# Performance work log

Measured on AMD Instinct MI355X. Metric: run time of the kernel, lower is better.

## Reference

```python
import jax, jax.numpy as jnp
import numpy as np

EMBED_DIM = 1024
NUM_HEADS = 16
HEAD_DIM = EMBED_DIM // NUM_HEADS
TGT_LEN, BSZ = 2048, 4


def setup_inputs() -> dict:
    key = jax.random.key(0)
    ks = jax.random.split(key, 12)
    s = 1.0 / np.sqrt(EMBED_DIM)
    inp = {
        "query": jax.random.normal(ks[0], (TGT_LEN, BSZ, EMBED_DIM), jnp.float32),
        "key": jax.random.normal(ks[1], (TGT_LEN, BSZ, EMBED_DIM), jnp.float32),
        "value": jax.random.normal(ks[2], (TGT_LEN, BSZ, EMBED_DIM), jnp.float32),
        # nn.Linear weights: [out, in], y = x @ W.T + b
        "Wq": jax.random.normal(ks[3], (EMBED_DIM, EMBED_DIM), jnp.float32) * s,
        "bq": jax.random.normal(ks[4], (EMBED_DIM,), jnp.float32) * s,
        "Wk": jax.random.normal(ks[5], (EMBED_DIM, EMBED_DIM), jnp.float32) * s,
        "bk": jax.random.normal(ks[6], (EMBED_DIM,), jnp.float32) * s,
        "Wv": jax.random.normal(ks[7], (EMBED_DIM, EMBED_DIM), jnp.float32) * s,
        "bv": jax.random.normal(ks[8], (EMBED_DIM,), jnp.float32) * s,
        "Wo": jax.random.normal(ks[9], (EMBED_DIM, EMBED_DIM), jnp.float32) * s,
        "bo": jax.random.normal(ks[10], (EMBED_DIM,), jnp.float32) * s,
    }
    return inp


def _split_heads(x, seq_len, bsz):
    # [S, B, E] -> [B*H, S, Dh]
    return x.reshape(seq_len, bsz * NUM_HEADS, HEAD_DIM).transpose(1, 0, 2)


def reference(query, key, value, Wq, bq, Wk, bk, Wv, bv, Wo, bo):
    tgt_len, bsz, embed_dim = query.shape
    src_len = key.shape[0]
    q = query @ Wq.T + bq
    k = key @ Wk.T + bk
    v = value @ Wv.T + bv
    q = _split_heads(q, tgt_len, bsz)   # [B*H, T, Dh]
    k = _split_heads(k, src_len, bsz)   # [B*H, S, Dh]
    v = _split_heads(v, src_len, bsz)   # [B*H, S, Dh]
    scale = 1.0 / np.sqrt(HEAD_DIM).astype(np.float32)
    attn_weights = jnp.einsum('btd,bsd->bts', q, k) * scale  # [B*H, T, S]
    attn_weights = jax.nn.softmax(attn_weights, axis=-1)
    attn = jnp.einsum('bts,bsd->btd', attn_weights, v)       # [B*H, T, Dh]
    attn = attn.transpose(1, 0, 2).reshape(tgt_len, bsz, embed_dim)
    return attn @ Wo.T + bo
```

## Files before the change

### kernel.cpp

```cpp
#include <hip/hip_runtime.h>
#include <stdint.h>

#define TGT 2048
#define BSZQ 4
#define EMB 1024
#define NHEAD 16
#define DH 64
#define BH 64
#define MROWS 8192

using short8 = __attribute__((ext_vector_type(8))) short;
using f32x4  = __attribute__((ext_vector_type(4))) float;
using u32x4  = __attribute__((ext_vector_type(4))) unsigned int;
typedef unsigned short u16;
typedef unsigned int u32;

#define QSCALE 0.18033688011112042f

__device__ __forceinline__ u16 f2bf(float f) {
  union { float f; u32 u; } v; v.f = f;
  return (u16)((v.u + 0x7fffu + ((v.u >> 16) & 1u)) >> 16);
}
__device__ __forceinline__ u32 packbf(float a, float b) {
  union { float f; u32 u; } x, y; x.f = a; y.f = b;
  return __builtin_amdgcn_perm(y.u + 0x8000u, x.u + 0x8000u, 0x07060302u);
}
__device__ __forceinline__ f32x4 mfma16(short8 a, short8 b, f32x4 c) {
  return __builtin_amdgcn_mfma_f32_16x16x32_bf16(a, b, c, 0, 0, 0);
}
__device__ __forceinline__ void gload_lds16(const u16* g, u16* l) {
  __builtin_amdgcn_global_load_lds((const __attribute__((address_space(1))) void*)g,
                                   (__attribute__((address_space(3))) void*)l,
                                   16, 0, 0);
}

__global__ __launch_bounds__(256)
void cvt3(const float* __restrict__ a, const float* __restrict__ b, const float* __restrict__ c,
          u16* __restrict__ oa, u16* __restrict__ ob, u16* __restrict__ oc)
{
  const float* s; u16* d;
  if (blockIdx.y == 0) { s = a; d = oa; }
  else if (blockIdx.y == 1) { s = b; d = ob; }
  else { s = c; d = oc; }
  const int i = (blockIdx.x * 256 + threadIdx.x) * 8;
  float4 v0 = *(const float4*)(s + i);
  float4 v1 = *(const float4*)(s + i + 4);
  union { u16 h[8]; short8 v; } r;
  r.h[0] = f2bf(v0.x); r.h[1] = f2bf(v0.y); r.h[2] = f2bf(v0.z); r.h[3] = f2bf(v0.w);
  r.h[4] = f2bf(v1.x); r.h[5] = f2bf(v1.y); r.h[6] = f2bf(v1.z); r.h[7] = f2bf(v1.w);
  *(short8*)(d + i) = r.v;
}
__global__ __launch_bounds__(256)
void cvt4(const float* __restrict__ a, const float* __restrict__ b,
          const float* __restrict__ c, const float* __restrict__ e,
          u16* __restrict__ oa, u16* __restrict__ ob, u16* __restrict__ oc, u16* __restrict__ oe)
{
  const float* s; u16* d;
  if (blockIdx.y == 0) { s = a; d = oa; }
  else if (blockIdx.y == 1) { s = b; d = ob; }
  else if (blockIdx.y == 2) { s = c; d = oc; }
  else { s = e; d = oe; }
  const int i = (blockIdx.x * 256 + threadIdx.x) * 8;
  float4 v0 = *(const float4*)(s + i);
  float4 v1 = *(const float4*)(s + i + 4);
  union { u16 h[8]; short8 v; } r;
  r.h[0] = f2bf(v0.x); r.h[1] = f2bf(v0.y); r.h[2] = f2bf(v0.z); r.h[3] = f2bf(v0.w);
  r.h[4] = f2bf(v1.x); r.h[5] = f2bf(v1.y); r.h[6] = f2bf(v1.z); r.h[7] = f2bf(v1.w);
  *(short8*)(d + i) = r.v;
}

__device__ __forceinline__
void gemm_body(const u16* __restrict__ A, const u16* __restrict__ W,
               const float* __restrict__ bias, void* __restrict__ outp,
               u16* As, u16* Bs, int mode)
{
  const int tid = threadIdx.x;
  const int wave = tid >> 6, lane = tid & 63;
  const int wm = wave >> 1, wn = wave & 1;
  const int col16 = lane & 15, quad = lane >> 4;
  const int m0 = blockIdx.y * 128, n0 = blockIdx.x * 128;
  const int lr = lane >> 2;
  const int lc = (lane & 3) * 8;

  f32x4 acc[4][4];
#pragma unroll
  for (int i = 0; i < 4; ++i)
#pragma unroll
    for (int j = 0; j < 4; ++j) acc[i][j] = (f32x4)0.0f;

  for (int kt = 0; kt < EMB / 64; ++kt) {
    const int k0 = kt * 64;
#pragma unroll
    for (int kk = 0; kk < 2; ++kk) {
#pragma unroll
      for (int h = 0; h < 2; ++h) {
        const int rbase = wave * 32 + h * 16;
        const int r = rbase + lr;
        gload_lds16(A + (size_t)(m0 + r) * EMB + k0 + kk * 32 + lc,
                    &As[kk * 4096 + rbase * 32]);
        gload_lds16(W + (size_t)(n0 + r) * EMB + k0 + kk * 32 + lc,
                    &Bs[kk * 4096 + rbase * 32]);
      }
    }
    __syncthreads();
    short8 af[4][2], bfr[4][2];
#pragma unroll
    for (int i = 0; i < 4; ++i)
#pragma unroll
      for (int kk = 0; kk < 2; ++kk) {
        af[i][kk]  = *(const short8*)&As[kk * 4096 + (wm * 64 + i * 16 + col16) * 32 + quad * 8];
        bfr[i][kk] = *(const short8*)&Bs[kk * 4096 + (wn * 64 + i * 16 + col16) * 32 + quad * 8];
      }
#pragma unroll
    for (int i = 0; i < 4; ++i)
#pragma unroll
      for (int j = 0; j < 4; ++j) {
        acc[i][j] = mfma16(af[i][0], bfr[j][0], acc[i][j]);
        acc[i][j] = mfma16(af[i][1], bfr[j][1], acc[i][j]);
      }
    __syncthreads();
  }

  const int rowb = quad * 4;
#pragma unroll
  for (int i = 0; i < 4; ++i) {
#pragma unroll
    for (int j = 0; j < 4; ++j) {
      const int gn = n0 + wn * 64 + j * 16 + col16;
      const float bia = bias[gn];
#pragma unroll
      for (int r = 0; r < 4; ++r) {
        const int gm = m0 + wm * 64 + i * 16 + rowb + r;
        float val = acc[i][j][r] + bia;
        const int t = gm >> 2, b = gm & 3, h = gn >> 6, d = gn & 63;
        if (mode == 0) {
          ((u16*)outp)[((size_t)(b * NHEAD + h) * TGT + t) * DH + d] = f2bf(val * QSCALE);
        } else if (mode == 1) {
          ((u16*)outp)[((size_t)(b * NHEAD + h) * TGT + t) * DH + d] = f2bf(val);
        } else if (mode == 2) {
          const int p = (t & ~127) + ((t & 15) << 3) + ((t >> 4) & 7);
          ((u16*)outp)[((size_t)(b * NHEAD + h) * DH + d) * TGT + p] = f2bf(val);
        } else {
          ((float*)outp)[(size_t)gm * EMB + gn] = val;
        }
      }
    }
  }
}

__global__ __launch_bounds__(256, 2)
void gemm_qkv(const u16* __restrict__ qb, const u16* __restrict__ kb, const u16* __restrict__ vb,
              const u16* __restrict__ wq, const u16* __restrict__ wk, const u16* __restrict__ wv,
              const float* __restrict__ bq, const float* __restrict__ bk, const float* __restrict__ bv,
              u16* __restrict__ qh, u16* __restrict__ kh, u16* __restrict__ vtp)
{
  __shared__ u16 As[2 * 4096];
  __shared__ u16 Bs[2 * 4096];
  const int z = blockIdx.z;
  const u16* A = (z == 0) ? qb : (z == 1) ? kb : vb;
  const u16* W = (z == 0) ? wq : (z == 1) ? wk : wv;
  const float* bias = (z == 0) ? bq : (z == 1) ? bk : bv;
  void* outp = (z == 0) ? (void*)qh : (z == 1) ? (void*)kh : (void*)vtp;
  gemm_body(A, W, bias, outp, As, Bs, z);
}

__global__ __launch_bounds__(256, 2)
void gemm_o(const u16* __restrict__ A, const u16* __restrict__ W,
            const float* __restrict__ bias, float* __restrict__ outp)
{
  __shared__ u16 As[2 * 4096];
  __shared__ u16 Bs[2 * 4096];
  gemm_body(A, W, bias, (void*)outp, As, Bs, 3);
}

__global__ __launch_bounds__(256, 2)
void flash_attn(const u16* __restrict__ qh, const u16* __restrict__ kh,
                const u16* __restrict__ vtp, u16* __restrict__ ao)
{
  __shared__ u16 Ks[128 * 64];
  __shared__ u16 Vs[64 * 128];
  __shared__ u16 Ps[128 * 136];

  const int tid = threadIdx.x;
  const int wave = tid >> 6, lane = tid & 63;
  const int col16 = lane & 15, quad = lane >> 4;
  const int id = blockIdx.x;
  const int bh = (id & 7) * 8 + (id >> 7);
  const int q0 = ((id >> 3) & 15) * 128;
  const int wq0 = q0 + wave * 32;

  const u16* qbase = qh + (size_t)bh * TGT * DH;
  const u16* kbase = kh + (size_t)bh * TGT * DH;
  const u16* vbase = vtp + (size_t)bh * DH * TGT;

  const int krl = lane >> 3;
  const int kgl = (lane & 7) ^ krl;
  const int vdl = wave * 4 + quad;
  const int vgl = (lane & 15) ^ vdl;

#define STAGE(S0) do { \
  _Pragma("unroll") for (int t_ = 0; t_ < 4; ++t_) { \
    gload_lds16(kbase + (size_t)((S0) + t_ * 32 + wave * 8 + krl) * DH + kgl * 8, \
                &Ks[(t_ * 32 + wave * 8) * 64]); \
    gload_lds16(vbase + (size_t)(t_ * 16 + vdl) * TGT + (S0) + vgl * 8, \
                &Vs[(t_ * 16 + wave * 4) * 128]); \
  } } while (0)

  short8 qf[2][2];
#pragma unroll
  for (int i = 0; i < 2; ++i)
#pragma unroll
    for (int kk = 0; kk < 2; ++kk)
      qf[i][kk] = *(const short8*)(qbase + (size_t)(wq0 + i * 16 + col16) * DH + kk * 32 + quad * 8);

  f32x4 oacc[2][4];
  float lsum[2][4];
#pragma unroll
  for (int i = 0; i < 2; ++i)
#pragma unroll
    for (int j = 0; j < 4; ++j) oacc[i][j] = (f32x4)0.0f;
#pragma unroll
  for (int i = 0; i < 2; ++i)
#pragma unroll
    for (int r = 0; r < 4; ++r) lsum[i][r] = 0.0f;

  STAGE(0);

  for (int st = 0; st < TGT / 128; ++st) {
    __syncthreads();

    u32x4 pk[2][4];
    const int kx = col16 & 7;
#pragma unroll
    for (int jp = 0; jp < 4; ++jp) {
      f32x4 s[2][2];
#pragma unroll
      for (int jh = 0; jh < 2; ++jh) {
        const int R = (jp * 2 + jh) * 16 + col16;
        short8 kf0 = *(const short8*)&Ks[R * 64 + ((quad ^ kx) << 3)];
        short8 kf1 = *(const short8*)&Ks[R * 64 + (((quad + 4) ^ kx) << 3)];
#pragma unroll
        for (int i = 0; i < 2; ++i) {
          f32x4 t0 = mfma16(qf[i][0], kf0, (f32x4)0.0f);
          s[i][jh] = mfma16(qf[i][1], kf1, t0);
        }
      }
#pragma unroll
      for (int i = 0; i < 2; ++i)
#pragma unroll
        for (int r = 0; r < 4; ++r) {
          float p0 = __builtin_amdgcn_exp2f(s[i][0][r]);
          float p1 = __builtin_amdgcn_exp2f(s[i][1][r]);
          lsum[i][r] += p0 + p1;
          pk[i][r][jp] = packbf(p0, p1);
        }
    }
#pragma unroll
    for (int i = 0; i < 2; ++i)
#pragma unroll
      for (int r = 0; r < 4; ++r)
        *(u32x4*)&Ps[(wave * 32 + i * 16 + quad * 4 + r) * 136 + col16 * 8] = pk[i][r];
#pragma unroll
    for (int ks = 0; ks < 4; ++ks) {
      short8 pf[2];
#pragma unroll
      for (int i = 0; i < 2; ++i)
        pf[i] = *(const short8*)&Ps[(wave * 32 + i * 16 + col16) * 136 + ks * 32 + quad * 8];
#pragma unroll
      for (int jd = 0; jd < 4; ++jd) {
        short8 vf = *(const short8*)&Vs[(jd * 16 + col16) * 128 + (((ks * 4 + quad) ^ col16) << 3)];
#pragma unroll
        for (int i = 0; i < 2; ++i)
          oacc[i][jd] = mfma16(pf[i], vf, oacc[i][jd]);
      }
    }
    __syncthreads();
    if (st < TGT / 128 - 1) STAGE((st + 1) * 128);
  }
#undef STAGE

#pragma unroll
  for (int i = 0; i < 2; ++i)
#pragma unroll
    for (int r = 0; r < 4; ++r) {
#pragma unroll
      for (int off = 1; off < 16; off <<= 1)
        lsum[i][r] += __shfl_xor(lsum[i][r], off, 64);
      lsum[i][r] = __builtin_amdgcn_rcpf(lsum[i][r]);
    }
  const int b = bh >> 4, h = bh & 15;
#pragma unroll
  for (int i = 0; i < 2; ++i)
#pragma unroll
    for (int jd = 0; jd < 4; ++jd)
#pragma unroll
      for (int r = 0; r < 4; ++r) {
        const int t = q0 + wave * 32 + i * 16 + quad * 4 + r;
        const int d = jd * 16 + col16;
        ao[((size_t)t * BSZQ + b) * EMB + h * DH + d] = f2bf(oacc[i][jd][r] * lsum[i][r]);
      }
}

extern "C" void kernel_launch(void* const* d_in, const int* in_sizes, int n_in,
                              void* d_out, int out_size, void* d_ws, size_t ws_size,
                              hipStream_t stream) {
  const float* query = (const float*)d_in[0];
  const float* key   = (const float*)d_in[1];
  const float* value = (const float*)d_in[2];
  const float* Wq = (const float*)d_in[3];
  const float* bq = (const float*)d_in[4];
  const float* Wk = (const float*)d_in[5];
  const float* bk = (const float*)d_in[6];
  const float* Wv = (const float*)d_in[7];
  const float* bv = (const float*)d_in[8];
  const float* Wo = (const float*)d_in[9];
  const float* bo = (const float*)d_in[10];

  const size_t BIG = (size_t)MROWS * EMB;
  const size_t WSZ = (size_t)EMB * EMB;
  u16* buf0 = (u16*)d_ws;
  u16* buf1 = buf0 + BIG;
  u16* buf2 = buf1 + BIG;
  u16* buf3 = buf2 + BIG;
  u16* wqb  = buf3 + BIG;
  u16* wkb  = wqb + WSZ;
  u16* wvb  = wkb + WSZ;
  u16* wob  = wvb + WSZ;

  cvt3<<<dim3(BIG / 2048, 3), 256, 0, stream>>>(query, key, value, buf0, buf1, buf2);
  cvt4<<<dim3(WSZ / 2048, 4), 256, 0, stream>>>(Wq, Wk, Wv, Wo, wqb, wkb, wvb, wob);

  gemm_qkv<<<dim3(EMB / 128, MROWS / 128, 3), 256, 0, stream>>>(
      buf0, buf1, buf2, wqb, wkb, wvb, bq, bk, bv,
      buf3 , buf0 , buf1 );

  flash_attn<<<1024, 256, 0, stream>>>(buf3, buf0, buf1, buf2);

  gemm_o<<<dim3(EMB / 128, MROWS / 128), 256, 0, stream>>>(buf2, wob, bo, (float*)d_out);
}
```

Before: 375.5 us.

## Double-buffer GEMM and attention LDS tiles and shrink GEMM tile to 128x64

The GEMM kernels now use a 128x64 output tile with swizzled 64-wide LDS rows. Their shared memory is double-buffered, so the next K slice is prefetched while MFMAs run, and only one barrier per iteration is needed. Flash attention also double-buffers its K and V tiles and processes each 128-key block in two 64-key halves with a smaller, XOR-swizzled P buffer, and the V-transpose permutation in the QKV epilogue is adjusted to match. The aim is to overlap global-to-LDS loads with compute and raise occupancy, at the cost of more LDS per block and lower per-block data reuse in the GEMMs.

```diff
diff --git a/kernel.cpp b/kernel.cpp
--- a/kernel.cpp
+++ b/kernel.cpp
@@ -11,7 +11,7 @@
 
 using short8 = __attribute__((ext_vector_type(8))) short;
 using f32x4  = __attribute__((ext_vector_type(4))) float;
-using u32x4  = __attribute__((ext_vector_type(4))) unsigned int;
+using u32x2  = __attribute__((ext_vector_type(2))) unsigned int;
 typedef unsigned short u16;
 typedef unsigned int u32;
 
@@ -76,69 +76,73 @@
 {
   const int tid = threadIdx.x;
   const int wave = tid >> 6, lane = tid & 63;
-  const int wm = wave >> 1, wn = wave & 1;
   const int col16 = lane & 15, quad = lane >> 4;
-  const int m0 = blockIdx.y * 128, n0 = blockIdx.x * 128;
-  const int lr = lane >> 2;
-  const int lc = (lane & 3) * 8;
-
-  f32x4 acc[4][4];
-#pragma unroll
-  for (int i = 0; i < 4; ++i)
+  const int m0 = blockIdx.y * 128, n0 = blockIdx.x * 64;
+  const int sr = lane >> 3;
+  const int sg = (lane & 7) ^ sr;
+  const int fk = col16 & 7;
+
+#define GSTAGE(K0, CB) do { \
+  _Pragma("unroll") for (int s_ = 0; s_ < 4; ++s_) \
+    gload_lds16(A + (size_t)(m0 + wave * 32 + s_ * 8 + sr) * EMB + (K0) + sg * 8, \
+                &As[(CB) * 8192 + (wave * 32 + s_ * 8) * 64]); \
+  _Pragma("unroll") for (int s_ = 0; s_ < 2; ++s_) \
+    gload_lds16(W + (size_t)(n0 + wave * 16 + s_ * 8 + sr) * EMB + (K0) + sg * 8, \
+                &Bs[(CB) * 4096 + (wave * 16 + s_ * 8) * 64]); \
+} while (0)
+
+  f32x4 acc[2][4];
+#pragma unroll
+  for (int i = 0; i < 2; ++i)
 #pragma unroll
     for (int j = 0; j < 4; ++j) acc[i][j] = (f32x4)0.0f;
 
+  GSTAGE(0, 0);
   for (int kt = 0; kt < EMB / 64; ++kt) {
-    const int k0 = kt * 64;
+    const int cb = kt & 1;
+    __syncthreads();
+    if (kt < EMB / 64 - 1) GSTAGE((kt + 1) * 64, cb ^ 1);
+    short8 af[2][2], bfr[4][2];
 #pragma unroll
     for (int kk = 0; kk < 2; ++kk) {
 #pragma unroll
-      for (int h = 0; h < 2; ++h) {
-        const int rbase = wave * 32 + h * 16;
-        const int r = rbase + lr;
-        gload_lds16(A + (size_t)(m0 + r) * EMB + k0 + kk * 32 + lc,
-                    &As[kk * 4096 + rbase * 32]);
-        gload_lds16(W + (size_t)(n0 + r) * EMB + k0 + kk * 32 + lc,
-                    &Bs[kk * 4096 + rbase * 32]);
-      }
+      for (int i = 0; i < 2; ++i)
+        af[i][kk] = *(const short8*)&As[cb * 8192 + (wave * 32 + i * 16 + col16) * 64
+                                        + (((kk * 4 + quad) ^ fk) << 3)];
+#pragma unroll
+      for (int j = 0; j < 4; ++j)
+        bfr[j][kk] = *(const short8*)&Bs[cb * 4096 + (j * 16 + col16) * 64
+                                         + (((kk * 4 + quad) ^ fk) << 3)];
     }
-    __syncthreads();
-    short8 af[4][2], bfr[4][2];
-#pragma unroll
-    for (int i = 0; i < 4; ++i)
-#pragma unroll
-      for (int kk = 0; kk < 2; ++kk) {
-        af[i][kk]  = *(const short8*)&As[kk * 4096 + (wm * 64 + i * 16 + col16) * 32 + quad * 8];
-        bfr[i][kk] = *(const short8*)&Bs[kk * 4096 + (wn * 64 + i * 16 + col16) * 32 + quad * 8];
-      }
-#pragma unroll
-    for (int i = 0; i < 4; ++i)
+#pragma unroll
+    for (int i = 0; i < 2; ++i)
 #pragma unroll
       for (int j = 0; j < 4; ++j) {
         acc[i][j] = mfma16(af[i][0], bfr[j][0], acc[i][j]);
         acc[i][j] = mfma16(af[i][1], bfr[j][1], acc[i][j]);
       }
-    __syncthreads();
   }
+#undef GSTAGE
 
   const int rowb = quad * 4;
 #pragma unroll
-  for (int i = 0; i < 4; ++i) {
+  for (int i = 0; i < 2; ++i) {
 #pragma unroll
     for (int j = 0; j < 4; ++j) {
-      const int gn = n0 + wn * 64 + j * 16 + col16;
+      const int gn = n0 + j * 16 + col16;
       const float bia = bias[gn];
+      const int h = gn >> 6, d = gn & 63;
 #pragma unroll
       for (int r = 0; r < 4; ++r) {
-        const int gm = m0 + wm * 64 + i * 16 + rowb + r;
+        const int gm = m0 + wave * 32 + i * 16 + rowb + r;
         float val = acc[i][j][r] + bia;
-        const int t = gm >> 2, b = gm & 3, h = gn >> 6, d = gn & 63;
+        const int t = gm >> 2, b = gm & 3;
         if (mode == 0) {
           ((u16*)outp)[((size_t)(b * NHEAD + h) * TGT + t) * DH + d] = f2bf(val * QSCALE);
         } else if (mode == 1) {
           ((u16*)outp)[((size_t)(b * NHEAD + h) * TGT + t) * DH + d] = f2bf(val);
         } else if (mode == 2) {
-          const int p = (t & ~127) + ((t & 15) << 3) + ((t >> 4) & 7);
+          const int p = (t & ~63) + ((t & 15) << 2) + ((t >> 4) & 3);
           ((u16*)outp)[((size_t)(b * NHEAD + h) * DH + d) * TGT + p] = f2bf(val);
         } else {
           ((float*)outp)[(size_t)gm * EMB + gn] = val;
@@ -148,13 +152,13 @@
   }
 }
 
-__global__ __launch_bounds__(256, 2)
+__global__ __launch_bounds__(256, 3)
 void gemm_qkv(const u16* __restrict__ qb, const u16* __restrict__ kb, const u16* __restrict__ vb,
               const u16* __restrict__ wq, const u16* __restrict__ wk, const u16* __restrict__ wv,
               const float* __restrict__ bq, const float* __restrict__ bk, const float* __restrict__ bv,
               u16* __restrict__ qh, u16* __restrict__ kh, u16* __restrict__ vtp)
 {
-  __shared__ u16 As[2 * 4096];
+  __shared__ u16 As[2 * 8192];
   __shared__ u16 Bs[2 * 4096];
   const int z = blockIdx.z;
   const u16* A = (z == 0) ? qb : (z == 1) ? kb : vb;
@@ -164,11 +168,11 @@
   gemm_body(A, W, bias, outp, As, Bs, z);
 }
 
-__global__ __launch_bounds__(256, 2)
+__global__ __launch_bounds__(256, 3)
 void gemm_o(const u16* __restrict__ A, const u16* __restrict__ W,
             const float* __restrict__ bias, float* __restrict__ outp)
 {
-  __shared__ u16 As[2 * 4096];
+  __shared__ u16 As[2 * 8192];
   __shared__ u16 Bs[2 * 4096];
   gemm_body(A, W, bias, (void*)outp, As, Bs, 3);
 }
@@ -177,9 +181,9 @@
 void flash_attn(const u16* __restrict__ qh, const u16* __restrict__ kh,
                 const u16* __restrict__ vtp, u16* __restrict__ ao)
 {
-  __shared__ u16 Ks[128 * 64];
-  __shared__ u16 Vs[64 * 128];
-  __shared__ u16 Ps[128 * 136];
+  __shared__ u16 Ks[2 * 128 * 64];
+  __shared__ u16 Vs[2 * 64 * 128];
+  __shared__ u16 Ps[128 * 64];
 
   const int tid = threadIdx.x;
   const int wave = tid >> 6, lane = tid & 63;
@@ -198,12 +202,12 @@
   const int vdl = wave * 4 + quad;
   const int vgl = (lane & 15) ^ vdl;
 
-#define STAGE(S0) do { \
+#define STAGE(S0, B) do { \
   _Pragma("unroll") for (int t_ = 0; t_ < 4; ++t_) { \
     gload_lds16(kbase + (size_t)((S0) + t_ * 32 + wave * 8 + krl) * DH + kgl * 8, \
-                &Ks[(t_ * 32 + wave * 8) * 64]); \
+                &Ks[(B) * 8192 + (t_ * 32 + wave * 8) * 64]); \
     gload_lds16(vbase + (size_t)(t_ * 16 + vdl) * TGT + (S0) + vgl * 8, \
-                &Vs[(t_ * 16 + wave * 4) * 128]); \
+                &Vs[(B) * 8192 + (t_ * 16 + wave * 4) * 128]); \
   } } while (0)
 
   short8 qf[2][2];
@@ -224,58 +228,68 @@
 #pragma unroll
     for (int r = 0; r < 4; ++r) lsum[i][r] = 0.0f;
 
-  STAGE(0);
+  STAGE(0, 0);
 
   for (int st = 0; st < TGT / 128; ++st) {
+    const int cb = st & 1;
     __syncthreads();
-
-    u32x4 pk[2][4];
-    const int kx = col16 & 7;
-#pragma unroll
-    for (int jp = 0; jp < 4; ++jp) {
-      f32x4 s[2][2];
-#pragma unroll
-      for (int jh = 0; jh < 2; ++jh) {
-        const int R = (jp * 2 + jh) * 16 + col16;
-        short8 kf0 = *(const short8*)&Ks[R * 64 + ((quad ^ kx) << 3)];
-        short8 kf1 = *(const short8*)&Ks[R * 64 + (((quad + 4) ^ kx) << 3)];
+    if (st < TGT / 128 - 1) STAGE((st + 1) * 128, cb ^ 1);
+
+#pragma unroll
+    for (int half = 0; half < 2; ++half) {
+      u32 pka[2][4][2];
+#pragma unroll
+      for (int jpL = 0; jpL < 2; ++jpL) {
+        f32x4 s[2][2];
+#pragma unroll
+        for (int jh = 0; jh < 2; ++jh) {
+          const int j = half * 4 + jpL * 2 + jh;
+          const int R = j * 16 + col16;
+          short8 kf0 = *(const short8*)&Ks[cb * 8192 + R * 64 + ((quad ^ (col16 & 7)) << 3)];
+          short8 kf1 = *(const short8*)&Ks[cb * 8192 + R * 64 + (((quad + 4) ^ (col16 & 7)) << 3)];
+#pragma unroll
+          for (int i = 0; i < 2; ++i) {
+            f32x4 t0 = mfma16(qf[i][0], kf0, (f32x4)0.0f);
+            s[i][jh] = mfma16(qf[i][1], kf1, t0);
+          }
+        }
+#pragma unroll
+        for (int i = 0; i < 2; ++i)
+#pragma unroll
+          for (int r = 0; r < 4; ++r) {
+            float p0 = __builtin_amdgcn_exp2f(s[i][0][r]);
+            float p1 = __builtin_amdgcn_exp2f(s[i][1][r]);
+            lsum[i][r] += p0 + p1;
+            pka[i][r][jpL] = packbf(p0, p1);
+          }
+      }
+#pragma unroll
+      for (int i = 0; i < 2; ++i)
+#pragma unroll
+        for (int r = 0; r < 4; ++r) {
+          const int row = wave * 32 + i * 16 + quad * 4 + r;
+          u32x2 w2; w2[0] = pka[i][r][0]; w2[1] = pka[i][r][1];
+          *(u32x2*)&Ps[row * 64 + (((col16 >> 1) ^ (row & 7)) << 3) + ((col16 & 1) << 2)] = w2;
+        }
+#pragma unroll
+      for (int ks = 0; ks < 2; ++ks) {
+        short8 pf[2];
 #pragma unroll
         for (int i = 0; i < 2; ++i) {
-          f32x4 t0 = mfma16(qf[i][0], kf0, (f32x4)0.0f);
-          s[i][jh] = mfma16(qf[i][1], kf1, t0);
-        }
-      }
-#pragma unroll
-      for (int i = 0; i < 2; ++i)
-#pragma unroll
-        for (int r = 0; r < 4; ++r) {
-          float p0 = __builtin_amdgcn_exp2f(s[i][0][r]);
-          float p1 = __builtin_amdgcn_exp2f(s[i][1][r]);
-          lsum[i][r] += p0 + p1;
-          pk[i][r][jp] = packbf(p0, p1);
-        }
+          const int row = wave * 32 + i * 16 + col16;
+          pf[i] = *(const short8*)&Ps[row * 64 + (((ks * 4 + quad) ^ (col16 & 7)) << 3)];
+        }
+#pragma unroll
+        for (int jd = 0; jd < 4; ++jd) {
+          const int d = jd * 16 + col16;
+          short8 vf = *(const short8*)&Vs[cb * 8192 + d * 128
+                                          + (((half * 8 + ks * 4 + quad) ^ col16) << 3)];
+#pragma unroll
+          for (int i = 0; i < 2; ++i)
+            oacc[i][jd] = mfma16(pf[i], vf, oacc[i][jd]);
+        }
+      }
     }
-#pragma unroll
-    for (int i = 0; i < 2; ++i)
-#pragma unroll
-      for (int r = 0; r < 4; ++r)
-        *(u32x4*)&Ps[(wave * 32 + i * 16 + quad * 4 + r) * 136 + col16 * 8] = pk[i][r];
-#pragma unroll
-    for (int ks = 0; ks < 4; ++ks) {
-      short8 pf[2];
-#pragma unroll
-      for (int i = 0; i < 2; ++i)
-        pf[i] = *(const short8*)&Ps[(wave * 32 + i * 16 + col16) * 136 + ks * 32 + quad * 8];
-#pragma unroll
-      for (int jd = 0; jd < 4; ++jd) {
-        short8 vf = *(const short8*)&Vs[(jd * 16 + col16) * 128 + (((ks * 4 + quad) ^ col16) << 3)];
-#pragma unroll
-        for (int i = 0; i < 2; ++i)
-          oacc[i][jd] = mfma16(pf[i], vf, oacc[i][jd]);
-      }
-    }
-    __syncthreads();
-    if (st < TGT / 128 - 1) STAGE((st + 1) * 128);
   }
 #undef STAGE
 
@@ -330,11 +344,11 @@
   cvt3<<<dim3(BIG / 2048, 3), 256, 0, stream>>>(query, key, value, buf0, buf1, buf2);
   cvt4<<<dim3(WSZ / 2048, 4), 256, 0, stream>>>(Wq, Wk, Wv, Wo, wqb, wkb, wvb, wob);
 
-  gemm_qkv<<<dim3(EMB / 128, MROWS / 128, 3), 256, 0, stream>>>(
+  gemm_qkv<<<dim3(EMB / 64, MROWS / 128, 3), 256, 0, stream>>>(
       buf0, buf1, buf2, wqb, wkb, wvb, bq, bk, bv,
       buf3 , buf0 , buf1 );
 
   flash_attn<<<1024, 256, 0, stream>>>(buf3, buf0, buf1, buf2);
 
-  gemm_o<<<dim3(EMB / 128, MROWS / 128), 256, 0, stream>>>(buf2, wob, bo, (float*)d_out);
-}
+  gemm_o<<<dim3(EMB / 64, MROWS / 128), 256, 0, stream>>>(buf2, wob, bo, (float*)d_out);
+}
```

Measured after the change: 374.6 us. About the same (-0.2%).
